# Optimization experiments

Hardware: AMD Instinct MI355X
Metric: run time of the kernel (lower is better)

## Reference

```python
import jax, jax.numpy as jnp
import numpy as np

BIG_NUMBER = 1e7   # repo constant used to mask padded adjacency slots
MAX_ITERS = 32     # params['flow_iters']


def _build_graph(B, N, D, valid_deg, seed=0):
    """Random d-regular-ish graph: each valid slot d holds a permutation of nodes,
    so every node has exactly `valid_deg` in-edges. in_indices[b,v,d] = (b,u,s)
    such that adj[b,u,s] == v. Padded slots (d >= valid_deg) hold the sentinel N
    and their in_indices point to a padded (near-zero-weight) flow entry."""
    rng = np.random.default_rng(seed)
    adj = np.full((B, N, D), N, dtype=np.int32)
    in_idx = np.zeros((B, N, D, 3), dtype=np.int32)
    in_idx[..., 0] = np.arange(B, dtype=np.int32)[:, None, None]
    in_idx[..., 2] = valid_deg  # padded slots -> flow[b, 0, valid_deg] (weight ~ 0)
    for b in range(B):
        for d in range(valid_deg):
            perm = rng.permutation(N).astype(np.int32)
            adj[b, :, d] = perm                      # edge u -> perm[u] via slot d
            inv = np.argsort(perm).astype(np.int32)  # inv[v] = u with perm[u] == v
            in_idx[b, :, d, 1] = inv
            in_idx[b, :, d, 2] = d
    return jnp.asarray(adj), jnp.asarray(in_idx)


def setup_inputs():
    B, N, D, VALID = 4, 100000, 16, 12
    key = jax.random.key(0)
    k1, k2 = jax.random.split(key)
    adj_lst, in_indices = _build_graph(B, N, D, VALID)
    return {
        "flow_proportions": jax.random.normal(k1, (B, N, D), dtype=jnp.float32),
        "demands": jax.random.normal(k2, (B, N, 1), dtype=jnp.float32),
        "adj_lst": adj_lst,
        "in_indices": in_indices,
        "num_nodes": N,
    }


def reference(flow_proportions, demands, adj_lst, in_indices, num_nodes):
    # --- masked softmax over neighbor slots (padded slots get -BIG_NUMBER) ---
    mask = (adj_lst == num_nodes).astype(flow_proportions.dtype)   # [B,N,D]
    masked = flow_proportions - BIG_NUMBER * mask
    weights = jax.nn.softmax(masked, axis=-1)                      # normalized_weights

    # --- mcf_solver: iterate flow <- weights * relu(inflow - demand) ---
    bidx = in_indices[..., 0]   # [B,N,D] batch index
    src = in_indices[..., 1]    # [B,N,D] source node of d-th in-edge
    slot = in_indices[..., 2]   # [B,N,D] slot of this node in source's adj list

    def step(flow, _):
        # gather incoming edge flows, sum -> inflow per node [B,N,1]
        inflow = flow[bidx, src, slot].sum(axis=-1, keepdims=True)
        new_flow = weights * jax.nn.relu(inflow - demands)
        return new_flow, None

    flow, _ = jax.lax.scan(step, jnp.zeros_like(weights), None, length=MAX_ITERS)
    # flow_cost (loss) = sum over nodes/slots of cost_fn(flow) = flow**2 here:
    # flow_cost = jnp.sum(flow * flow, axis=(1, 2))
    return flow
```

## Files before the change

### kernel.cpp

```cpp
#include <hip/hip_runtime.h>

#define DEG 16
#define MAX_ITERS 32
#define BLK_F 1024

__device__ __forceinline__ void grid_barrier(unsigned* cnt, unsigned* gen,
                                             unsigned target, unsigned nblocks) {
    __syncthreads();
    if (threadIdx.x == 0) {
        __threadfence();
        unsigned arrived = __hip_atomic_fetch_add(cnt, 1u, __ATOMIC_ACQ_REL,
                                                  __HIP_MEMORY_SCOPE_AGENT);
        if (arrived == nblocks - 1u) {
            __hip_atomic_store(cnt, 0u, __ATOMIC_RELAXED, __HIP_MEMORY_SCOPE_AGENT);
            __hip_atomic_fetch_add(gen, 1u, __ATOMIC_RELEASE, __HIP_MEMORY_SCOPE_AGENT);
        } else {
            while (__hip_atomic_load(gen, __ATOMIC_RELAXED,
                                     __HIP_MEMORY_SCOPE_AGENT) < target) {
                __builtin_amdgcn_s_sleep(16);
            }
        }
        __threadfence();
    }
    __syncthreads();
}

__device__ __forceinline__ void softmax_row(const float* __restrict__ fp,
                                            const int* __restrict__ adj,
                                            float* __restrict__ wout,
                                            size_t base, int N) {
    const float4* f4 = (const float4*)(fp + base);
    const int4*   a4 = (const int4*)(adj + base);
    float v[DEG];
#pragma unroll
    for (int k = 0; k < DEG / 4; ++k) {
        float4 f = f4[k];
        int4   a = a4[k];
        v[4*k+0] = (a.x == N) ? f.x - 1e7f : f.x;
        v[4*k+1] = (a.y == N) ? f.y - 1e7f : f.y;
        v[4*k+2] = (a.z == N) ? f.z - 1e7f : f.z;
        v[4*k+3] = (a.w == N) ? f.w - 1e7f : f.w;
    }
    float m = v[0];
#pragma unroll
    for (int j = 1; j < DEG; ++j) m = fmaxf(m, v[j]);
    float s = 0.f;
#pragma unroll
    for (int j = 0; j < DEG; ++j) { v[j] = __expf(v[j] - m); s += v[j]; }
    float inv = 1.f / s;
    float4* w4 = (float4*)(wout + base);
#pragma unroll
    for (int k = 0; k < DEG / 4; ++k) {
        float4 o;
        o.x = v[4*k+0] * inv;
        o.y = v[4*k+1] * inv;
        o.z = v[4*k+2] * inv;
        o.w = v[4*k+3] * inv;
        w4[k] = o;
    }
}

__global__ __launch_bounds__(BLK_F, 4)
void fused2_k(const float* __restrict__ fp, const int* __restrict__ adj,
              const int* __restrict__ in_idx, const float* __restrict__ dem,
              const int* __restrict__ nn, float* __restrict__ wout,
              float* __restrict__ Ra, float* __restrict__ Rb,
              unsigned* __restrict__ bar_cnt, unsigned* __restrict__ bar_gen,
              int nodes) {
    const int tid = blockIdx.x * blockDim.x + threadIdx.x;
    const int T = gridDim.x * blockDim.x;
    const int N = *nn;
    const unsigned nb = gridDim.x;
    unsigned bar = 0;

    const int  n0 = tid, n1 = tid + T;
    const bool a0 = (n0 < nodes), a1 = (n1 < nodes);
    const size_t b0 = (size_t)n0 * DEG, b1 = (size_t)n1 * DEG;

    if (a0) softmax_row(fp, adj, wout, b0, N);
    if (a1) softmax_row(fp, adj, wout, b1, N);
    grid_barrier(bar_cnt, bar_gen, ++bar, nb);

    int   src0[DEG], src1[DEG];
    float w0[DEG],   w1[DEG];
    float d0 = 0.f, d1 = 0.f;
    unsigned skipA = 0, skipB = 0;
    if (a0) {
        d0 = dem[n0];
        const int* t = in_idx + 3 * b0;
#pragma unroll
        for (int k = 0; k < DEG; ++k) {
            int fi = t[3*k] * N + t[3*k + 1];
            src0[k] = fi;
            w0[k]   = wout[(size_t)fi * DEG + t[3*k + 2]];
        }
    } else {
#pragma unroll
        for (int k = 0; k < DEG; ++k) { src0[k] = 0; w0[k] = 0.f; }
    }
    if (a1) {
        d1 = dem[n1];
        const int* t = in_idx + 3 * b1;
#pragma unroll
        for (int k = 0; k < DEG; ++k) {
            int fi = t[3*k] * N + t[3*k + 1];
            src1[k] = fi;
            w1[k]   = wout[(size_t)fi * DEG + t[3*k + 2]];
        }
    } else {
#pragma unroll
        for (int k = 0; k < DEG; ++k) { src1[k] = 0; w1[k] = 0.f; }
    }
#pragma unroll
    for (int k = 0; k < DEG; ++k) {
        if (__ballot(w0[k] != 0.f) == 0ull) skipA |= (1u << k);
        if (__ballot(w1[k] != 0.f) == 0ull) skipB |= (1u << k);
    }
    const unsigned sk0 = __builtin_amdgcn_readfirstlane(skipA);
    const unsigned sk1 = __builtin_amdgcn_readfirstlane(skipB);

    float r0 = fmaxf(-d0, 0.f), r1 = fmaxf(-d1, 0.f);
    if (a0) Ra[n0] = r0;
    if (a1) Ra[n1] = r1;
    grid_barrier(bar_cnt, bar_gen, ++bar, nb);

    const float* Rin = Ra;
    float*       Rout = Rb;
    for (int t = 1; t < MAX_ITERS; ++t) {
        float acc0 = 0.f, acc1 = 0.f;
#pragma unroll
        for (int k = 0; k < DEG; ++k) {
            if (!((sk0 >> k) & 1u) && a0) acc0 += w0[k] * Rin[src0[k]];
            if (!((sk1 >> k) & 1u) && a1) acc1 += w1[k] * Rin[src1[k]];
        }
        r0 = fmaxf(acc0 - d0, 0.f);
        r1 = fmaxf(acc1 - d1, 0.f);
        if (t < MAX_ITERS - 1) {
            if (a0) Rout[n0] = r0;
            if (a1) Rout[n1] = r1;
            grid_barrier(bar_cnt, bar_gen, ++bar, nb);
            float* tmp = (float*)Rin; Rin = Rout; Rout = tmp;
        }
    }

    if (a0) {
        float4* w4 = (float4*)(wout + b0);
#pragma unroll
        for (int k = 0; k < DEG / 4; ++k) {
            float4 v = w4[k];
            v.x *= r0; v.y *= r0; v.z *= r0; v.w *= r0;
            w4[k] = v;
        }
    }
    if (a1) {
        float4* w4 = (float4*)(wout + b1);
#pragma unroll
        for (int k = 0; k < DEG / 4; ++k) {
            float4 v = w4[k];
            v.x *= r1; v.y *= r1; v.z *= r1; v.w *= r1;
            w4[k] = v;
        }
    }
}

__global__ void softmax_k(const float* __restrict__ fp, const int* __restrict__ adj,
                          const int* __restrict__ nn, float* __restrict__ wout,
                          int nodes) {
    int i = blockIdx.x * blockDim.x + threadIdx.x;
    if (i >= nodes) return;
    softmax_row(fp, adj, wout, (size_t)i * DEG, *nn);
}

__global__ void gather_k(const int* __restrict__ in_idx, const float* __restrict__ w,
                         const int* __restrict__ nn, int* __restrict__ e_src,
                         float* __restrict__ e_w, int edges) {
    int e = blockIdx.x * blockDim.x + threadIdx.x;
    if (e >= edges) return;
    const int N = *nn;
    size_t e3 = 3 * (size_t)e;
    int fi = in_idx[e3] * N + in_idx[e3 + 1];
    e_src[e] = fi;
    e_w[e]   = w[(size_t)fi * DEG + in_idx[e3 + 2]];
}

__global__ void iter_k(const int* __restrict__ e_src, const float* __restrict__ e_w,
                       const float* __restrict__ dem, const float* __restrict__ Rin,
                       float* __restrict__ Rout, int nodes) {
    int i = blockIdx.x * blockDim.x + threadIdx.x;
    if (i >= nodes) return;
    const size_t base = (size_t)i * DEG;
    const int4*   s4 = (const int4*)(e_src + base);
    const float4* w4 = (const float4*)(e_w + base);
    float acc = 0.f;
#pragma unroll
    for (int k = 0; k < DEG / 4; ++k) {
        int4   s = s4[k];
        float4 w = w4[k];
        acc += w.x * Rin[s.x];
        acc += w.y * Rin[s.y];
        acc += w.z * Rin[s.z];
        acc += w.w * Rin[s.w];
    }
    float r = acc - dem[i];
    Rout[i] = r > 0.f ? r : 0.f;
}

__global__ void final_k(const float* __restrict__ w, const float* __restrict__ R,
                        float* __restrict__ out, int nodes) {
    int i = blockIdx.x * blockDim.x + threadIdx.x;
    if (i >= nodes) return;
    float r = R[i];
    const size_t base = (size_t)i * DEG;
    const float4* w4 = (const float4*)(w + base);
    float4* o4 = (float4*)(out + base);
#pragma unroll
    for (int k = 0; k < DEG / 4; ++k) {
        float4 v = w4[k];
        v.x *= r; v.y *= r; v.z *= r; v.w *= r;
        o4[k] = v;
    }
}

extern "C" void kernel_launch(void* const* d_in, const int* in_sizes, int n_in,
                              void* d_out, int out_size, void* d_ws, size_t ws_size,
                              hipStream_t stream) {
    const float* fp  = (const float*)d_in[0];
    const float* dem = (const float*)d_in[1];
    const int*   adj = (const int*)d_in[2];
    const int*   idx = (const int*)d_in[3];
    const int*   nn  = (const int*)d_in[4];

    const int edges = in_sizes[0];
    const int nodes = in_sizes[1];

    float* weights = (float*)d_out;

    char* ws = (char*)d_ws;
    unsigned* bar_cnt = (unsigned*)ws;
    unsigned* bar_gen = (unsigned*)(ws + 128);
    int*   e_src = (int*)ws;
    float* e_w   = (float*)(ws + (size_t)edges * sizeof(int));
    float* R0    = (float*)(ws + (size_t)edges * sizeof(int) + (size_t)edges * sizeof(float));
    float* R1    = R0 + nodes;

    const int threads_needed = (nodes + 1) / 2;
    const int gf = (threads_needed + BLK_F - 1) / BLK_F;

    int dev = 0, cus = 0, maxBlk = 0;
    hipGetDevice(&dev);
    hipDeviceGetAttribute(&cus, hipDeviceAttributeMultiprocessorCount, dev);
    hipOccupancyMaxActiveBlocksPerMultiprocessor(&maxBlk, (const void*)fused2_k,
                                                 BLK_F, 0);

    if ((long long)maxBlk * cus >= gf) {
        hipMemsetAsync(ws, 0, 256, stream);
        void* args[] = { (void*)&fp, (void*)&adj, (void*)&idx, (void*)&dem,
                         (void*)&nn, (void*)&weights, (void*)&R0, (void*)&R1,
                         (void*)&bar_cnt, (void*)&bar_gen, (void*)&nodes };
        hipLaunchCooperativeKernel((const void*)fused2_k, dim3(gf), dim3(BLK_F),
                                   args, 0, stream);
    } else {
        const int blk = 256;
        const int gn = (nodes + blk - 1) / blk;
        const int ge = (edges + blk - 1) / blk;
        hipMemsetAsync(R0, 0, (size_t)nodes * sizeof(float), stream);
        softmax_k<<<gn, blk, 0, stream>>>(fp, adj, nn, weights, nodes);
        gather_k<<<ge, blk, 0, stream>>>(idx, weights, nn, e_src, e_w, edges);
        float* a = R0;
        float* b = R1;
        for (int t = 0; t < MAX_ITERS; ++t) {
            iter_k<<<gn, blk, 0, stream>>>(e_src, e_w, dem, a, b, nodes);
            float* tmp = a; a = b; b = tmp;
        }
        final_k<<<gn, blk, 0, stream>>>(weights, a, (float*)d_out, nodes);
    }
}
```

Before: 1.028 ms.

## Fix cooperative grid to 256 blocks with batch-aware XCD node partitioning

The cooperative kernel now runs on a fixed grid of 256 blocks. Each block owns a contiguous node range, and in the 4-batch case blocks are mapped so that each batch's nodes sit on a consistent subset of block IDs, likely to keep gathers local to one XCD's L2. It also cuts the barrier spin sleep, loads in_indices as int4 vectors, and splits the per-slot accumulation loop by active flag. This aims to reduce L2 misses on the irregular gathers and lower barrier latency, at the cost of depending on the hardware's block-to-XCD assignment and adding more spin traffic.

Measured after the change: 1.029 ms. About the same (+0.1%).

```diff
diff --git a/kernel.cpp b/kernel.cpp
--- a/kernel.cpp
+++ b/kernel.cpp
@@ -3,6 +3,7 @@
 #define DEG 16
 #define MAX_ITERS 32
 #define BLK_F 1024
+#define GRID_F 256
 
 __device__ __forceinline__ void grid_barrier(unsigned* cnt, unsigned* gen,
                                              unsigned target, unsigned nblocks) {
@@ -17,7 +18,7 @@
         } else {
             while (__hip_atomic_load(gen, __ATOMIC_RELAXED,
                                      __HIP_MEMORY_SCOPE_AGENT) < target) {
-                __builtin_amdgcn_s_sleep(16);
+                __builtin_amdgcn_s_sleep(2);
             }
         }
         __threadfence();
@@ -60,21 +61,64 @@
     }
 }
 
+__device__ __forceinline__ void load_edges(const int* __restrict__ in_idx,
+                                           const float* __restrict__ wsrc,
+                                           int n, int N,
+                                           int* __restrict__ src,
+                                           float* __restrict__ w) {
+    const int4* t4 = (const int4*)(in_idx + 3 * (size_t)n * DEG);
+#pragma unroll
+    for (int g = 0; g < 4; ++g) {
+        int4 qa = t4[3*g + 0];
+        int4 qb = t4[3*g + 1];
+        int4 qc = t4[3*g + 2];
+        int b0 = qa.x, s0 = qa.y, l0 = qa.z;
+        int b1 = qa.w, s1 = qb.x, l1 = qb.y;
+        int b2 = qb.z, s2 = qb.w, l2 = qc.x;
+        int b3 = qc.y, s3 = qc.z, l3 = qc.w;
+        int f0 = b0 * N + s0, f1 = b1 * N + s1;
+        int f2 = b2 * N + s2, f3 = b3 * N + s3;
+        src[4*g+0] = f0; src[4*g+1] = f1; src[4*g+2] = f2; src[4*g+3] = f3;
+        w[4*g+0] = wsrc[(size_t)f0 * DEG + l0];
+        w[4*g+1] = wsrc[(size_t)f1 * DEG + l1];
+        w[4*g+2] = wsrc[(size_t)f2 * DEG + l2];
+        w[4*g+3] = wsrc[(size_t)f3 * DEG + l3];
+    }
+}
+
 __global__ __launch_bounds__(BLK_F, 4)
-void fused2_k(const float* __restrict__ fp, const int* __restrict__ adj,
+void fused3_k(const float* __restrict__ fp, const int* __restrict__ adj,
               const int* __restrict__ in_idx, const float* __restrict__ dem,
               const int* __restrict__ nn, float* __restrict__ wout,
               float* __restrict__ Ra, float* __restrict__ Rb,
               unsigned* __restrict__ bar_cnt, unsigned* __restrict__ bar_gen,
               int nodes) {
-    const int tid = blockIdx.x * blockDim.x + threadIdx.x;
-    const int T = gridDim.x * blockDim.x;
     const int N = *nn;
     const unsigned nb = gridDim.x;
     unsigned bar = 0;
 
-    const int  n0 = tid, n1 = tid + T;
-    const bool a0 = (n0 < nodes), a1 = (n1 < nodes);
+    int start, end;
+    if (nodes == 4 * N && nb == GRID_F) {
+        int batch = (blockIdx.x & 7) >> 1;
+        int rank  = ((blockIdx.x >> 3) << 1) | (blockIdx.x & 1);
+        int per   = (N + 63) >> 6;
+        int bend  = batch * N + N;
+        start = batch * N + rank * per;
+        end   = start + per;
+        if (end > bend) end = bend;
+        if (start > bend) start = bend;
+    } else {
+        int per = (nodes + nb - 1) / nb;
+        start = blockIdx.x * per;
+        end   = start + per;
+        if (end > nodes) end = nodes;
+        if (start > nodes) start = nodes;
+    }
+
+    const int n0 = start + (int)threadIdx.x;
+    const int n1 = start + (int)threadIdx.x + BLK_F;
+    const bool a0 = (n0 < end);
+    const bool a1 = (n1 < end);
     const size_t b0 = (size_t)n0 * DEG, b1 = (size_t)n1 * DEG;
 
     if (a0) softmax_row(fp, adj, wout, b0, N);
@@ -84,33 +128,12 @@
     int   src0[DEG], src1[DEG];
     float w0[DEG],   w1[DEG];
     float d0 = 0.f, d1 = 0.f;
+#pragma unroll
+    for (int k = 0; k < DEG; ++k) { src0[k] = 0; w0[k] = 0.f; src1[k] = 0; w1[k] = 0.f; }
+    if (a0) { d0 = dem[n0]; load_edges(in_idx, wout, n0, N, src0, w0); }
+    if (a1) { d1 = dem[n1]; load_edges(in_idx, wout, n1, N, src1, w1); }
+
     unsigned skipA = 0, skipB = 0;
-    if (a0) {
-        d0 = dem[n0];
-        const int* t = in_idx + 3 * b0;
-#pragma unroll
-        for (int k = 0; k < DEG; ++k) {
-            int fi = t[3*k] * N + t[3*k + 1];
-            src0[k] = fi;
-            w0[k]   = wout[(size_t)fi * DEG + t[3*k + 2]];
-        }
-    } else {
-#pragma unroll
-        for (int k = 0; k < DEG; ++k) { src0[k] = 0; w0[k] = 0.f; }
-    }
-    if (a1) {
-        d1 = dem[n1];
-        const int* t = in_idx + 3 * b1;
-#pragma unroll
-        for (int k = 0; k < DEG; ++k) {
-            int fi = t[3*k] * N + t[3*k + 1];
-            src1[k] = fi;
-            w1[k]   = wout[(size_t)fi * DEG + t[3*k + 2]];
-        }
-    } else {
-#pragma unroll
-        for (int k = 0; k < DEG; ++k) { src1[k] = 0; w1[k] = 0.f; }
-    }
 #pragma unroll
     for (int k = 0; k < DEG; ++k) {
         if (__ballot(w0[k] != 0.f) == 0ull) skipA |= (1u << k);
@@ -128,10 +151,15 @@
     float*       Rout = Rb;
     for (int t = 1; t < MAX_ITERS; ++t) {
         float acc0 = 0.f, acc1 = 0.f;
-#pragma unroll
-        for (int k = 0; k < DEG; ++k) {
-            if (!((sk0 >> k) & 1u) && a0) acc0 += w0[k] * Rin[src0[k]];
-            if (!((sk1 >> k) & 1u) && a1) acc1 += w1[k] * Rin[src1[k]];
+        if (a0) {
+#pragma unroll
+            for (int k = 0; k < DEG; ++k)
+                if (!((sk0 >> k) & 1u)) acc0 += w0[k] * Rin[src0[k]];
+        }
+        if (a1) {
+#pragma unroll
+            for (int k = 0; k < DEG; ++k)
+                if (!((sk1 >> k) & 1u)) acc1 += w1[k] * Rin[src1[k]];
         }
         r0 = fmaxf(acc0 - d0, 0.f);
         r1 = fmaxf(acc1 - d1, 0.f);
@@ -243,21 +271,20 @@
     float* R0    = (float*)(ws + (size_t)edges * sizeof(int) + (size_t)edges * sizeof(float));
     float* R1    = R0 + nodes;
 
-    const int threads_needed = (nodes + 1) / 2;
-    const int gf = (threads_needed + BLK_F - 1) / BLK_F;
-
     int dev = 0, cus = 0, maxBlk = 0;
     hipGetDevice(&dev);
     hipDeviceGetAttribute(&cus, hipDeviceAttributeMultiprocessorCount, dev);
-    hipOccupancyMaxActiveBlocksPerMultiprocessor(&maxBlk, (const void*)fused2_k,
+    hipOccupancyMaxActiveBlocksPerMultiprocessor(&maxBlk, (const void*)fused3_k,
                                                  BLK_F, 0);
 
-    if ((long long)maxBlk * cus >= gf) {
+    const int per_blk = (nodes + GRID_F - 1) / GRID_F;
+
+    if (maxBlk >= 1 && cus >= GRID_F && per_blk <= 2 * BLK_F) {
         hipMemsetAsync(ws, 0, 256, stream);
         void* args[] = { (void*)&fp, (void*)&adj, (void*)&idx, (void*)&dem,
                          (void*)&nn, (void*)&weights, (void*)&R0, (void*)&R1,
                          (void*)&bar_cnt, (void*)&bar_gen, (void*)&nodes };
-        hipLaunchCooperativeKernel((const void*)fused2_k, dim3(gf), dim3(BLK_F),
+        hipLaunchCooperativeKernel((const void*)fused3_k, dim3(GRID_F), dim3(BLK_F),
                                    args, 0, stream);
     } else {
         const int blk = 256;
```

## Partition iterations per XCD with local barriers and compact 12-edge lists

Applied to the files above, without the earlier changes.

Restructures the fused cooperative kernel so that each batch's graph is handled by blocks on a pair of XCDs, each keeping its own copy of R, with XCD-scoped barriers replacing grid-wide barriers for the 31 propagation iterations. It also compacts the in-edge lists to 12 real edges per node, storing precomputed source indices and weights, so the padded slots are never loaded. The aim is to cut cross-die synchronisation latency and gather traffic. In exchange it adds runtime checks that fall back to a grid-barrier path when the structure assumptions fail, relies on reading the hardware XCC id and on the block-to-XCD distribution, and spins with a shorter sleep.

New measurement: 1.025 ms. Within noise of the previous version (-0.3%).

```diff
diff --git a/kernel.cpp b/kernel.cpp
--- a/kernel.cpp
+++ b/kernel.cpp
@@ -1,8 +1,25 @@
 #include <hip/hip_runtime.h>
 
 #define DEG 16
+#define E12 12
 #define MAX_ITERS 32
-#define BLK_F 1024
+#define BLK 1024
+
+__device__ __forceinline__ float ld_sc0(const float* p) {
+    return __hip_atomic_load(p, __ATOMIC_RELAXED, __HIP_MEMORY_SCOPE_AGENT);
+}
+__device__ __forceinline__ void st_sc0(float* p, float v) {
+    __hip_atomic_store(p, v, __ATOMIC_RELAXED, __HIP_MEMORY_SCOPE_AGENT);
+}
+__device__ __forceinline__ unsigned ld_u32_sc0(const unsigned* p) {
+    return __hip_atomic_load(p, __ATOMIC_RELAXED, __HIP_MEMORY_SCOPE_AGENT);
+}
+
+__device__ __forceinline__ int get_xcd() {
+    unsigned x;
+    asm volatile("s_getreg_b32 %0, hwreg(HW_REG_XCC_ID)" : "=s"(x));
+    return (int)(x & 7u);
+}
 
 __device__ __forceinline__ void grid_barrier(unsigned* cnt, unsigned* gen,
                                              unsigned target, unsigned nblocks) {
@@ -16,11 +33,29 @@
             __hip_atomic_fetch_add(gen, 1u, __ATOMIC_RELEASE, __HIP_MEMORY_SCOPE_AGENT);
         } else {
             while (__hip_atomic_load(gen, __ATOMIC_RELAXED,
-                                     __HIP_MEMORY_SCOPE_AGENT) < target) {
-                __builtin_amdgcn_s_sleep(16);
-            }
+                                     __HIP_MEMORY_SCOPE_AGENT) < target)
+                __builtin_amdgcn_s_sleep(2);
         }
         __threadfence();
+    }
+    __syncthreads();
+}
+
+__device__ __forceinline__ void xcd_barrier(unsigned* cnt, unsigned* gen,
+                                            unsigned target, unsigned nblocks) {
+    __syncthreads();
+    if (threadIdx.x == 0) {
+        unsigned arrived = __hip_atomic_fetch_add(cnt, 1u, __ATOMIC_RELEASE,
+                                                  __HIP_MEMORY_SCOPE_WORKGROUP);
+        if (arrived == nblocks - 1u) {
+            __hip_atomic_store(cnt, 0u, __ATOMIC_RELAXED,
+                               __HIP_MEMORY_SCOPE_WORKGROUP);
+            __hip_atomic_fetch_add(gen, 1u, __ATOMIC_RELEASE,
+                                   __HIP_MEMORY_SCOPE_WORKGROUP);
+        } else {
+            while (ld_u32_sc0(gen) < target)
+                __builtin_amdgcn_s_sleep(2);
+        }
     }
     __syncthreads();
 }
@@ -60,105 +95,246 @@
     }
 }
 
-__global__ __launch_bounds__(BLK_F, 4)
-void fused2_k(const float* __restrict__ fp, const int* __restrict__ adj,
+__device__ __forceinline__ float node_acc_sc0(const int* __restrict__ es,
+                                              const float* __restrict__ ew,
+                                              const float* __restrict__ Rc) {
+    const int4*   s4 = (const int4*)es;
+    const float4* w4 = (const float4*)ew;
+    int4 a = s4[0], b = s4[1], c = s4[2];
+    float4 x = w4[0], y = w4[1], z = w4[2];
+    float acc;
+    acc  = x.x * ld_sc0(Rc + a.x);
+    acc += x.y * ld_sc0(Rc + a.y);
+    acc += x.z * ld_sc0(Rc + a.z);
+    acc += x.w * ld_sc0(Rc + a.w);
+    acc += y.x * ld_sc0(Rc + b.x);
+    acc += y.y * ld_sc0(Rc + b.y);
+    acc += y.z * ld_sc0(Rc + b.z);
+    acc += y.w * ld_sc0(Rc + b.w);
+    acc += z.x * ld_sc0(Rc + c.x);
+    acc += z.y * ld_sc0(Rc + c.y);
+    acc += z.z * ld_sc0(Rc + c.z);
+    acc += z.w * ld_sc0(Rc + c.w);
+    return acc;
+}
+
+__device__ __forceinline__ float node_acc_plain(const int* __restrict__ es,
+                                                const float* __restrict__ ew,
+                                                const float* __restrict__ Rc) {
+    const int4*   s4 = (const int4*)es;
+    const float4* w4 = (const float4*)ew;
+    int4 a = s4[0], b = s4[1], c = s4[2];
+    float4 x = w4[0], y = w4[1], z = w4[2];
+    float acc;
+    acc  = x.x * Rc[a.x];
+    acc += x.y * Rc[a.y];
+    acc += x.z * Rc[a.z];
+    acc += x.w * Rc[a.w];
+    acc += y.x * Rc[b.x];
+    acc += y.y * Rc[b.y];
+    acc += y.z * Rc[b.z];
+    acc += y.w * Rc[b.w];
+    acc += z.x * Rc[c.x];
+    acc += z.y * Rc[c.y];
+    acc += z.z * Rc[c.z];
+    acc += z.w * Rc[c.w];
+    return acc;
+}
+
+__global__ __launch_bounds__(BLK, 8)
+void fused6_k(const float* __restrict__ fp, const int* __restrict__ adj,
               const int* __restrict__ in_idx, const float* __restrict__ dem,
               const int* __restrict__ nn, float* __restrict__ wout,
-              float* __restrict__ Ra, float* __restrict__ Rb,
-              unsigned* __restrict__ bar_cnt, unsigned* __restrict__ bar_gen,
-              int nodes) {
-    const int tid = blockIdx.x * blockDim.x + threadIdx.x;
-    const int T = gridDim.x * blockDim.x;
-    const int N = *nn;
-    const unsigned nb = gridDim.x;
-    unsigned bar = 0;
-
-    const int  n0 = tid, n1 = tid + T;
-    const bool a0 = (n0 < nodes), a1 = (n1 < nodes);
-    const size_t b0 = (size_t)n0 * DEG, b1 = (size_t)n1 * DEG;
-
-    if (a0) softmax_row(fp, adj, wout, b0, N);
-    if (a1) softmax_row(fp, adj, wout, b1, N);
-    grid_barrier(bar_cnt, bar_gen, ++bar, nb);
-
-    int   src0[DEG], src1[DEG];
-    float w0[DEG],   w1[DEG];
-    float d0 = 0.f, d1 = 0.f;
-    unsigned skipA = 0, skipB = 0;
-    if (a0) {
-        d0 = dem[n0];
-        const int* t = in_idx + 3 * b0;
-#pragma unroll
-        for (int k = 0; k < DEG; ++k) {
-            int fi = t[3*k] * N + t[3*k + 1];
-            src0[k] = fi;
-            w0[k]   = wout[(size_t)fi * DEG + t[3*k + 2]];
+              char* __restrict__ wsb, int nodes) {
+    unsigned* g_cnt   = (unsigned*)(wsb);
+    unsigned* g_gen   = (unsigned*)(wsb + 128);
+    unsigned* blkcnt  = (unsigned*)(wsb + 2304);
+    unsigned* ovf     = (unsigned*)(wsb + 2432);
+    int*   e_src  = (int*)(wsb + 4096);
+    float* e_w    = (float*)(wsb + 4096 + (size_t)E12 * nodes * 4);
+    float* slices = e_w + (size_t)E12 * nodes;
+    float* Rf     = slices + 4 * (size_t)nodes;
+
+    const int N  = *nn;
+    const int Nb = N;
+    const unsigned nblocks = gridDim.x;
+    const int tid = (int)threadIdx.x;
+
+    __shared__ int sh_xcd, sh_rank, sh_mode, sh_K;
+    unsigned gb = 0;
+
+    if (tid == 0) {
+        int x = get_xcd();
+        sh_xcd  = x;
+        sh_rank = (int)__hip_atomic_fetch_add(&blkcnt[x], 1u, __ATOMIC_RELAXED,
+                                              __HIP_MEMORY_SCOPE_AGENT);
+    }
+    __syncthreads();
+    const int my_xcd  = sh_xcd;
+    const int my_rank = sh_rank;
+
+    {
+        int g = (int)blockIdx.x * BLK + tid;
+        if (g < nodes) softmax_row(fp, adj, wout, (size_t)g * DEG, N);
+    }
+    grid_barrier(g_cnt, g_gen, ++gb, nblocks);
+
+    if (tid == 0) {
+        const int need = (Nb + 2 * BLK - 1) / (2 * BLK);
+        unsigned c[8];
+#pragma unroll
+        for (int x = 0; x < 8; ++x) c[x] = ld_u32_sc0(&blkcnt[x]);
+        bool ok = (4 * Nb == nodes) && (Nb > 0);
+#pragma unroll
+        for (int b = 0; b < 4; ++b)
+            ok = ok && (c[2*b] >= (unsigned)need || c[2*b+1] >= (unsigned)need);
+        sh_mode = ok ? 1 : 0;
+        sh_K    = (int)c[my_xcd];
+    }
+    __syncthreads();
+
+    {
+        int g = (int)blockIdx.x * BLK + tid;
+        if (g < nodes) {
+            const int4* t4 = (const int4*)(in_idx + 3 * (size_t)g * DEG);
+            int   cs[DEG]; float cw[DEG]; int cb[DEG];
+#pragma unroll
+            for (int q = 0; q < 4; ++q) {
+                int4 qa = t4[3*q + 0];
+                int4 qb = t4[3*q + 1];
+                int4 qc = t4[3*q + 2];
+                cb[4*q+0] = qa.x; cs[4*q+0] = qa.y; int l0 = qa.z;
+                cb[4*q+1] = qa.w; cs[4*q+1] = qb.x; int l1 = qb.y;
+                cb[4*q+2] = qb.z; cs[4*q+2] = qb.w; int l2 = qc.x;
+                cb[4*q+3] = qc.y; cs[4*q+3] = qc.z; int l3 = qc.w;
+                cw[4*q+0] = wout[((size_t)(cb[4*q+0]) * Nb + cs[4*q+0]) * DEG + l0];
+                cw[4*q+1] = wout[((size_t)(cb[4*q+1]) * Nb + cs[4*q+1]) * DEG + l1];
+                cw[4*q+2] = wout[((size_t)(cb[4*q+2]) * Nb + cs[4*q+2]) * DEG + l2];
+                cw[4*q+3] = wout[((size_t)(cb[4*q+3]) * Nb + cs[4*q+3]) * DEG + l3];
+            }
+            const int gbatch = g / Nb;
+            bool bad = (cw[12] != 0.f) || (cw[13] != 0.f) ||
+                       (cw[14] != 0.f) || (cw[15] != 0.f);
+#pragma unroll
+            for (int k = 0; k < E12; ++k) bad = bad || (cb[k] != gbatch);
+            if (bad)
+                __hip_atomic_store(ovf, 1u, __ATOMIC_RELAXED,
+                                   __HIP_MEMORY_SCOPE_AGENT);
+            int4*   es4 = (int4*)(e_src + (size_t)g * E12);
+            float4* ew4 = (float4*)(e_w + (size_t)g * E12);
+            es4[0] = make_int4(cs[0], cs[1], cs[2], cs[3]);
+            es4[1] = make_int4(cs[4], cs[5], cs[6], cs[7]);
+            es4[2] = make_int4(cs[8], cs[9], cs[10], cs[11]);
+            ew4[0] = make_float4(cw[0], cw[1], cw[2], cw[3]);
+            ew4[1] = make_float4(cw[4], cw[5], cw[6], cw[7]);
+            ew4[2] = make_float4(cw[8], cw[9], cw[10], cw[11]);
+        }
+    }
+    grid_barrier(g_cnt, g_gen, ++gb, nblocks);
+
+    if (tid == 0) {
+        if (ld_u32_sc0(ovf) != 0u) sh_mode = 0;
+    }
+    __syncthreads();
+    const bool fast = (sh_mode == 1);
+
+    if (fast) {
+        const int need = (Nb + 2 * BLK - 1) / (2 * BLK);
+        const int K = sh_K;
+        if (K < need) return;
+
+        const int batch = my_xcd >> 1;
+        const int bbase = batch * Nb;
+        const int base  = my_rank * (2 * BLK);
+        const int l0 = base + tid;
+        const int l1 = base + tid + BLK;
+        const bool a0 = (l0 < Nb), a1 = (l1 < Nb);
+        const int g0 = bbase + l0, g1 = bbase + l1;
+
+        unsigned* xc = (unsigned*)(wsb + 256 + my_xcd * 256);
+        unsigned* xg = (unsigned*)(wsb + 256 + my_xcd * 256 + 128);
+        unsigned xb = 0;
+
+        float* R0s = slices + (size_t)(my_xcd * 2 + 0) * Nb;
+        float* R1s = slices + (size_t)(my_xcd * 2 + 1) * Nb;
+
+        float d0 = a0 ? dem[g0] : 0.f;
+        float d1 = a1 ? dem[g1] : 0.f;
+
+        float r0 = fmaxf(-d0, 0.f), r1 = fmaxf(-d1, 0.f);
+        if (a0) st_sc0(R0s + l0, r0);
+        if (a1) st_sc0(R1s + l1, r1);
+        if (a0) st_sc0(R1s + l0, r0);
+        if (a1) st_sc0(R0s + l1, r1);
+        xcd_barrier(xc, xg, ++xb, (unsigned)K);
+
+        const float* Rc = R0s;
+        float*       Rn = R1s;
+        const int* es0 = e_src + (size_t)g0 * E12;
+        const int* es1 = e_src + (size_t)g1 * E12;
+        const float* ew0 = e_w + (size_t)g0 * E12;
+        const float* ew1 = e_w + (size_t)g1 * E12;
+
+        for (int t = 1; t < MAX_ITERS; ++t) {
+            if (a0) r0 = fmaxf(node_acc_sc0(es0, ew0, Rc) - d0, 0.f);
+            if (a1) r1 = fmaxf(node_acc_sc0(es1, ew1, Rc) - d1, 0.f);
+            if (t < MAX_ITERS - 1) {
+                if (a0) st_sc0(Rn + l0, r0);
+                if (a1) st_sc0(Rn + l1, r1);
+                xcd_barrier(xc, xg, ++xb, (unsigned)K);
+                const float* tmp = Rc; Rc = Rn; Rn = (float*)tmp;
+            }
+        }
+
+        if (a0) {
+            float4* w4 = (float4*)(wout + (size_t)g0 * DEG);
+#pragma unroll
+            for (int k = 0; k < DEG / 4; ++k) {
+                float4 v = w4[k];
+                v.x *= r0; v.y *= r0; v.z *= r0; v.w *= r0;
+                w4[k] = v;
+            }
+        }
+        if (a1) {
+            float4* w4 = (float4*)(wout + (size_t)g1 * DEG);
+#pragma unroll
+            for (int k = 0; k < DEG / 4; ++k) {
+                float4 v = w4[k];
+                v.x *= r1; v.y *= r1; v.z *= r1; v.w *= r1;
+                w4[k] = v;
+            }
         }
     } else {
-#pragma unroll
-        for (int k = 0; k < DEG; ++k) { src0[k] = 0; w0[k] = 0.f; }
-    }
-    if (a1) {
-        d1 = dem[n1];
-        const int* t = in_idx + 3 * b1;
-#pragma unroll
-        for (int k = 0; k < DEG; ++k) {
-            int fi = t[3*k] * N + t[3*k + 1];
-            src1[k] = fi;
-            w1[k]   = wout[(size_t)fi * DEG + t[3*k + 2]];
-        }
-    } else {
-#pragma unroll
-        for (int k = 0; k < DEG; ++k) { src1[k] = 0; w1[k] = 0.f; }
-    }
-#pragma unroll
-    for (int k = 0; k < DEG; ++k) {
-        if (__ballot(w0[k] != 0.f) == 0ull) skipA |= (1u << k);
-        if (__ballot(w1[k] != 0.f) == 0ull) skipB |= (1u << k);
-    }
-    const unsigned sk0 = __builtin_amdgcn_readfirstlane(skipA);
-    const unsigned sk1 = __builtin_amdgcn_readfirstlane(skipB);
-
-    float r0 = fmaxf(-d0, 0.f), r1 = fmaxf(-d1, 0.f);
-    if (a0) Ra[n0] = r0;
-    if (a1) Ra[n1] = r1;
-    grid_barrier(bar_cnt, bar_gen, ++bar, nb);
-
-    const float* Rin = Ra;
-    float*       Rout = Rb;
-    for (int t = 1; t < MAX_ITERS; ++t) {
-        float acc0 = 0.f, acc1 = 0.f;
-#pragma unroll
-        for (int k = 0; k < DEG; ++k) {
-            if (!((sk0 >> k) & 1u) && a0) acc0 += w0[k] * Rin[src0[k]];
-            if (!((sk1 >> k) & 1u) && a1) acc1 += w1[k] * Rin[src1[k]];
-        }
-        r0 = fmaxf(acc0 - d0, 0.f);
-        r1 = fmaxf(acc1 - d1, 0.f);
-        if (t < MAX_ITERS - 1) {
-            if (a0) Rout[n0] = r0;
-            if (a1) Rout[n1] = r1;
-            grid_barrier(bar_cnt, bar_gen, ++bar, nb);
-            float* tmp = (float*)Rin; Rin = Rout; Rout = tmp;
-        }
-    }
-
-    if (a0) {
-        float4* w4 = (float4*)(wout + b0);
-#pragma unroll
-        for (int k = 0; k < DEG / 4; ++k) {
-            float4 v = w4[k];
-            v.x *= r0; v.y *= r0; v.z *= r0; v.w *= r0;
-            w4[k] = v;
-        }
-    }
-    if (a1) {
-        float4* w4 = (float4*)(wout + b1);
-#pragma unroll
-        for (int k = 0; k < DEG / 4; ++k) {
-            float4 v = w4[k];
-            v.x *= r1; v.y *= r1; v.z *= r1; v.w *= r1;
-            w4[k] = v;
+        const int g = (int)blockIdx.x * BLK + tid;
+        const bool act = (g < nodes);
+        int gbbase = 0;
+        float d = 0.f;
+        if (act) { gbbase = (g / Nb) * Nb; d = dem[g]; }
+        const int*   es = e_src + (size_t)g * E12;
+        const float* ew = e_w + (size_t)g * E12;
+
+        float r = fmaxf(-d, 0.f);
+        if (act) Rf[g] = r;
+        grid_barrier(g_cnt, g_gen, ++gb, nblocks);
+
+        const float* Rc = Rf;
+        float*       Rn = Rf + nodes;
+        for (int t = 1; t < MAX_ITERS; ++t) {
+            if (act) r = fmaxf(node_acc_plain(es, ew, Rc + gbbase) - d, 0.f);
+            if (t < MAX_ITERS - 1) {
+                if (act) Rn[g] = r;
+                grid_barrier(g_cnt, g_gen, ++gb, nblocks);
+                const float* tmp = Rc; Rc = Rn; Rn = (float*)tmp;
+            }
+        }
+        if (act) {
+            float4* w4 = (float4*)(wout + (size_t)g * DEG);
+#pragma unroll
+            for (int k = 0; k < DEG / 4; ++k) {
+                float4 v = w4[k];
+                v.x *= r; v.y *= r; v.z *= r; v.w *= r;
+                w4[k] = v;
+            }
         }
     }
 }
@@ -172,25 +348,25 @@
 }
 
 __global__ void gather_k(const int* __restrict__ in_idx, const float* __restrict__ w,
-                         const int* __restrict__ nn, int* __restrict__ e_src,
-                         float* __restrict__ e_w, int edges) {
+                         const int* __restrict__ nn, int* __restrict__ e_srcO,
+                         float* __restrict__ e_wO, int edges) {
     int e = blockIdx.x * blockDim.x + threadIdx.x;
     if (e >= edges) return;
     const int N = *nn;
     size_t e3 = 3 * (size_t)e;
     int fi = in_idx[e3] * N + in_idx[e3 + 1];
-    e_src[e] = fi;
-    e_w[e]   = w[(size_t)fi * DEG + in_idx[e3 + 2]];
-}
-
-__global__ void iter_k(const int* __restrict__ e_src, const float* __restrict__ e_w,
+    e_srcO[e] = fi;
+    e_wO[e]   = w[(size_t)fi * DEG + in_idx[e3 + 2]];
+}
+
+__global__ void iter_k(const int* __restrict__ e_srcO, const float* __restrict__ e_wO,
                        const float* __restrict__ dem, const float* __restrict__ Rin,
                        float* __restrict__ Rout, int nodes) {
     int i = blockIdx.x * blockDim.x + threadIdx.x;
     if (i >= nodes) return;
     const size_t base = (size_t)i * DEG;
-    const int4*   s4 = (const int4*)(e_src + base);
-    const float4* w4 = (const float4*)(e_w + base);
+    const int4*   s4 = (const int4*)(e_srcO + base);
+    const float4* w4 = (const float4*)(e_wO + base);
     float acc = 0.f;
 #pragma unroll
     for (int k = 0; k < DEG / 4; ++k) {
@@ -234,42 +410,43 @@
     const int nodes = in_sizes[1];
 
     float* weights = (float*)d_out;
-
-    char* ws = (char*)d_ws;
-    unsigned* bar_cnt = (unsigned*)ws;
-    unsigned* bar_gen = (unsigned*)(ws + 128);
-    int*   e_src = (int*)ws;
-    float* e_w   = (float*)(ws + (size_t)edges * sizeof(int));
-    float* R0    = (float*)(ws + (size_t)edges * sizeof(int) + (size_t)edges * sizeof(float));
-    float* R1    = R0 + nodes;
-
-    const int threads_needed = (nodes + 1) / 2;
-    const int gf = (threads_needed + BLK_F - 1) / BLK_F;
+    char*  ws      = (char*)d_ws;
 
     int dev = 0, cus = 0, maxBlk = 0;
     hipGetDevice(&dev);
     hipDeviceGetAttribute(&cus, hipDeviceAttributeMultiprocessorCount, dev);
-    hipOccupancyMaxActiveBlocksPerMultiprocessor(&maxBlk, (const void*)fused2_k,
-                                                 BLK_F, 0);
-
-    if ((long long)maxBlk * cus >= gf) {
-        hipMemsetAsync(ws, 0, 256, stream);
+    hipOccupancyMaxActiveBlocksPerMultiprocessor(&maxBlk, (const void*)fused6_k,
+                                                 BLK, 0);
+
+    const int grid = 2 * cus;
+    const size_t ws_need = 4096 + (size_t)nodes * (E12 * 8 + 16 + 8);
+
+    const bool fused_ok = (maxBlk >= 2) &&
+                          ((long long)grid * BLK >= nodes) &&
+                          (ws_size >= ws_need) &&
+                          (nodes % 4 == 0);
+
+    if (fused_ok) {
+        hipMemsetAsync(ws, 0, 4096, stream);
         void* args[] = { (void*)&fp, (void*)&adj, (void*)&idx, (void*)&dem,
-                         (void*)&nn, (void*)&weights, (void*)&R0, (void*)&R1,
-                         (void*)&bar_cnt, (void*)&bar_gen, (void*)&nodes };
-        hipLaunchCooperativeKernel((const void*)fused2_k, dim3(gf), dim3(BLK_F),
+                         (void*)&nn, (void*)&weights, (void*)&ws, (void*)&nodes };
+        hipLaunchCooperativeKernel((const void*)fused6_k, dim3(grid), dim3(BLK),
                                    args, 0, stream);
     } else {
+        int*   e_srcO = (int*)ws;
+        float* e_wO   = (float*)(ws + (size_t)edges * sizeof(int));
+        float* R0     = (float*)(ws + (size_t)edges * 8);
+        float* R1     = R0 + nodes;
         const int blk = 256;
         const int gn = (nodes + blk - 1) / blk;
         const int ge = (edges + blk - 1) / blk;
         hipMemsetAsync(R0, 0, (size_t)nodes * sizeof(float), stream);
         softmax_k<<<gn, blk, 0, stream>>>(fp, adj, nn, weights, nodes);
-        gather_k<<<ge, blk, 0, stream>>>(idx, weights, nn, e_src, e_w, edges);
+        gather_k<<<ge, blk, 0, stream>>>(idx, weights, nn, e_srcO, e_wO, edges);
         float* a = R0;
         float* b = R1;
         for (int t = 0; t < MAX_ITERS; ++t) {
-            iter_k<<<gn, blk, 0, stream>>>(e_src, e_w, dem, a, b, nodes);
+            iter_k<<<gn, blk, 0, stream>>>(e_srcO, e_wO, dem, a, b, nodes);
             float* tmp = a; a = b; b = tmp;
         }
         final_k<<<gn, blk, 0, stream>>>(weights, a, (float*)d_out, nodes);
```
